# Kernel tuning notes

Hardware: AMD Instinct MI355X
Metric: run time of the kernel (lower is better)

Reference implementation:

```python
import jax, jax.numpy as jnp
import numpy as np

BN_EPS = 1e-5
C = 128  # channels (hardcoded by feed_forward convs)


def _bn(v, gamma, beta, mean, var):
    # BatchNorm1d in inference form over channel axis of [B, C, N]
    scale = gamma / jnp.sqrt(var + BN_EPS)
    return (v - mean[:, None]) * scale[:, None] + beta[:, None]


def setup_inputs() -> dict:
    key = jax.random.key(0)
    ks = jax.random.split(key, 8)
    B, N = 8, 2048
    s = 0.05
    return {
        "x": jax.random.normal(ks[0], (B, N, C), jnp.float32),
        "Wq": jax.random.normal(ks[1], (C // 4, C), jnp.float32) * s,
        "Wk": jax.random.normal(ks[2], (C // 4, C), jnp.float32) * s,
        "Wv": jax.random.normal(ks[3], (C, C), jnp.float32) * s,
        "bv": jnp.zeros((C,), jnp.float32),
        "Wt": jax.random.normal(ks[4], (C, C), jnp.float32) * s,
        "bt": jnp.zeros((C,), jnp.float32),
        "g1": jnp.ones((C,), jnp.float32),
        "b1": jnp.zeros((C,), jnp.float32),
        "m1": jnp.zeros((C,), jnp.float32),
        "v1": jnp.ones((C,), jnp.float32),
        "W1": jax.random.normal(ks[5], (512, C), jnp.float32) * s,
        "bf1": jnp.zeros((512,), jnp.float32),
        "W2": jax.random.normal(ks[6], (C, 512), jnp.float32) * s,
        "bf2": jnp.zeros((C,), jnp.float32),
        "g2": jnp.ones((C,), jnp.float32),
        "b2": jnp.zeros((C,), jnp.float32),
        "m2": jnp.zeros((C,), jnp.float32),
        "v2": jnp.ones((C,), jnp.float32),
    }


def reference(x, Wq, Wk, Wv, bv, Wt, bt, g1, b1, m1, v1,
              W1, bf1, W2, bf2, g2, b2, m2, v2):
    # x: [B, N, C] -> work in [B, C, N] layout like the torch module
    xc = jnp.transpose(x, (0, 2, 1))                      # [B, C, N]
    # q_conv(x).permute -> [B, N, C/4]; k_conv -> [B, C/4, N]
    x_q = jnp.einsum('bnc,oc->bno', x, Wq)                # [B, N, C/4]
    x_k = jnp.einsum('bnc,oc->bon', x, Wk)                # [B, C/4, N]
    x_v = jnp.einsum('bnc,oc->bon', x, Wv) + bv[:, None]  # [B, C, N]

    energy = jnp.einsum('bnd,bdm->bnm', x_q, x_k)         # [B, N, N]
    scale = jnp.sqrt(jnp.asarray(C, x.dtype))             # sqrt(x_v.shape[-2])
    attention = jax.nn.softmax(energy / scale, axis=-1)   # [B, N, N]
    x_r = jnp.einsum('bcn,bnm->bcm', x_v, attention)      # [B, C, N]

    t = jnp.einsum('oc,bcn->bon', Wt, xc - x_r) + bt[:, None]
    x_r2 = jax.nn.relu(_bn(t, g1, b1, m1, v1))
    h = xc + x_r2                                         # [B, C, N]

    residual = h
    f = jax.nn.relu(jnp.einsum('oc,bcn->bon', W1, h) + bf1[:, None])
    f = jnp.einsum('of,bfn->bon', W2, f) + bf2[:, None]
    out = _bn(residual + f, g2, b2, m2, v2)               # [B, C, N]
    return jnp.transpose(out, (0, 2, 1))                  # [B, N, C]
```

## Files before the change

kernel.cpp:

```cpp
#include <hip/hip_runtime.h>
#include <hip/hip_bf16.h>

#define BDIM 256
#define NPTS (8 * 2048)
#define CC 128
#define DD 32
#define FF 512
#define NN 2048
#define SCALE 0.08838834764831845f

typedef float f32x4 __attribute__((ext_vector_type(4)));
typedef short s16x8 __attribute__((ext_vector_type(8)));
typedef unsigned short ushort_t;

__device__ __forceinline__ ushort_t bf16r(float x) {
    __hip_bfloat16 h = __float2bfloat16(x);
    return *reinterpret_cast<ushort_t*>(&h);
}
__device__ __forceinline__ float bf16tof(ushort_t u) {
    unsigned v = ((unsigned)u) << 16;
    return *reinterpret_cast<float*>(&v);
}
__device__ __forceinline__ unsigned pack2(float a, float b) {
    return ((unsigned)bf16r(b) << 16) | (unsigned)bf16r(a);
}

__global__ void k_cvt_all(const float* __restrict__ W1, const float* __restrict__ W2,
                          const float* __restrict__ Wq, const float* __restrict__ Wk,
                          const float* __restrict__ Wv, const float* __restrict__ Wt,
                          ushort_t* __restrict__ dst) {
    int i = blockIdx.x * BDIM + threadIdx.x;
    const float* src; int off;
    if (i < 16384)      { src = W1; off = 0; }
    else if (i < 32768) { src = W2; off = 16384; }
    else if (i < 33792) { src = Wq; off = 32768; }
    else if (i < 34816) { src = Wk; off = 33792; }
    else if (i < 38912) { src = Wv; off = 34816; }
    else                { src = Wt; off = 38912; }
    float4 v = ((const float4*)src)[i - off];
    *(uint2*)(dst + (long)i * 4) = make_uint2(pack2(v.x, v.y), pack2(v.z, v.w));
}

__global__ __launch_bounds__(256) void k_proj(
        const float* __restrict__ x, const ushort_t* __restrict__ Wb,
        const float* __restrict__ bv,
        ushort_t* __restrict__ qg, ushort_t* __restrict__ kg,
        ushort_t* __restrict__ vTg) {
    __shared__ ushort_t xs[32][136];
    __shared__ ushort_t qks[32][72];
    __shared__ ushort_t vs[32][136];
    int b = blockIdx.x & 7;
    int n0 = (blockIdx.x >> 3) * 32;
    long base = (long)b * NN + n0;
    int t = threadIdx.x, w = t >> 6, l = t & 63, a = l & 15, g = l >> 4;
    {
        const float4* xg4 = (const float4*)(x + base * CC);
        #pragma unroll
        for (int rep = 0; rep < 4; ++rep) {
            int i = rep * BDIM + t;
            float4 v4 = xg4[i];
            int p = i >> 5, c4 = (i & 31) * 4;
            *(uint2*)&xs[p][c4] = make_uint2(pack2(v4.x, v4.y), pack2(v4.z, v4.w));
        }
    }
    s16x8 bF[3][4];
    #pragma unroll
    for (int ct = 0; ct < 3; ++ct) {
        int ctg = w * 3 + ct;
        #pragma unroll
        for (int ki = 0; ki < 4; ++ki)
            bF[ct][ki] = *(const s16x8*)(Wb + ((long)(ctg * 16 + a)) * CC + ki * 32 + g * 8);
    }
    __syncthreads();
    #pragma unroll
    for (int rt = 0; rt < 2; ++rt) {
        s16x8 aF[4];
        #pragma unroll
        for (int ki = 0; ki < 4; ++ki)
            aF[ki] = *(const s16x8*)&xs[rt * 16 + a][ki * 32 + g * 8];
        #pragma unroll
        for (int ct = 0; ct < 3; ++ct) {
            f32x4 acc = (f32x4){0.f, 0.f, 0.f, 0.f};
            #pragma unroll
            for (int ki = 0; ki < 4; ++ki)
                acc = __builtin_amdgcn_mfma_f32_16x16x32_bf16(aF[ki], bF[ct][ki], acc, 0, 0, 0);
            int ctg = w * 3 + ct;
            int oc = ctg * 16 + a;
            float bias = (oc >= 64) ? bv[oc - 64] : 0.f;
            #pragma unroll
            for (int r = 0; r < 4; ++r) {
                int p = rt * 16 + g * 4 + r;
                float val = acc[r] + bias;
                if (oc < 64) qks[p][oc] = bf16r(val);
                else         vs[p][oc - 64] = bf16r(val);
            }
        }
    }
    __syncthreads();
    {
        int p = t >> 3, c = (t & 7) * 4;
        *(uint2*)(qg + (base + p) * DD + c) = *(const uint2*)&qks[p][c];
        *(uint2*)(kg + (base + p) * DD + c) = *(const uint2*)&qks[p][32 + c];
    }
    #pragma unroll
    for (int rep = 0; rep < 2; ++rep) {
        int i = rep * BDIM + t;
        int c = i & 127, nch = i >> 7;
        int p0 = nch * 8;
        uint4 r;
        r.x = (unsigned)vs[p0+0][c] | ((unsigned)vs[p0+1][c] << 16);
        r.y = (unsigned)vs[p0+2][c] | ((unsigned)vs[p0+3][c] << 16);
        r.z = (unsigned)vs[p0+4][c] | ((unsigned)vs[p0+5][c] << 16);
        r.w = (unsigned)vs[p0+6][c] | ((unsigned)vs[p0+7][c] << 16);
        *(uint4*)(vTg + ((long)(b * CC + c)) * NN + n0 + p0) = r;
    }
}

__global__ __launch_bounds__(256) void k_rowstats(
        const ushort_t* __restrict__ qg, const ushort_t* __restrict__ kg,
        float* __restrict__ rowinv) {
    __shared__ float ps[4][64];
    int b = blockIdx.x & 7;
    int nt = (blockIdx.x >> 3) * 64;
    int t = threadIdx.x, w = t >> 6, l = t & 63, a = l & 15, g = l >> 4;
    s16x8 qA[4];
    #pragma unroll
    for (int s = 0; s < 4; ++s)
        qA[s] = *(const s16x8*)(qg + ((long)(b * NN + nt + s*16 + a)) * DD + g*8);
    float sm[16];
    #pragma unroll
    for (int i = 0; i < 16; ++i) sm[i] = 0.f;
    s16x8 kB = *(const s16x8*)(kg + ((long)(b * NN + w * 16 + a)) * DD + g*8);
    for (int it = 0; it < 32; ++it) {
        s16x8 kBn;
        if (it < 31)
            kBn = *(const s16x8*)(kg + ((long)(b * NN + ((it+1)*4 + w)*16 + a)) * DD + g*8);
        #pragma unroll
        for (int s = 0; s < 4; ++s) {
            f32x4 D = (f32x4){0.f, 0.f, 0.f, 0.f};
            D = __builtin_amdgcn_mfma_f32_16x16x32_bf16(qA[s], kB, D, 0, 0, 0);
            #pragma unroll
            for (int r = 0; r < 4; ++r)
                sm[s * 4 + r] += __expf(D[r] * SCALE);
        }
        kB = kBn;
    }
    #pragma unroll
    for (int off = 1; off < 16; off <<= 1)
        #pragma unroll
        for (int ix = 0; ix < 16; ++ix)
            sm[ix] += __shfl_xor(sm[ix], off, 64);
    if (a == 0) {
        #pragma unroll
        for (int s = 0; s < 4; ++s)
            #pragma unroll
            for (int r = 0; r < 4; ++r)
                ps[w][s * 16 + g * 4 + r] = sm[s * 4 + r];
    }
    __syncthreads();
    if (t < 64) {
        float S = ps[0][t] + ps[1][t] + ps[2][t] + ps[3][t];
        rowinv[(long)b * NN + nt + t] = 1.f / S;
    }
}

__global__ __launch_bounds__(512) void k_pv(
        const ushort_t* __restrict__ qg, const ushort_t* __restrict__ kg,
        const ushort_t* __restrict__ vTg, const float* __restrict__ rowinv,
        const float* __restrict__ x, const ushort_t* __restrict__ Wtb,
        const float* __restrict__ bt,
        const float* __restrict__ g1, const float* __restrict__ b1,
        const float* __restrict__ m1, const float* __restrict__ v1,
        ushort_t* __restrict__ hb) {
    __shared__ __align__(16) char arena[17408];
    auto pT = (ushort_t (*)[32][72])(arena);
    int b = blockIdx.x & 7;
    int m0 = (blockIdx.x >> 3) * 32;
    int t = threadIdx.x, w = t >> 6, l = t & 63, a = l & 15, g = l >> 4;
    int nsub = w & 3, msub = w >> 2;
    const ushort_t* vTb = vTg + (long)b * CC * NN;
    s16x8 kf = *(const s16x8*)(kg + ((long)(b * NN + m0 + msub * 16 + a)) * DD + g * 8);
    const ushort_t* qrow = qg + ((long)(b * NN + nsub * 16 + a)) * DD + g * 8;
    const float*    rrow = rowinv + (long)b * NN + nsub * 16 + g * 4;
    int c = w * 16 + a;
    const ushort_t* vrow = vTb + (long)c * NN + g * 8;
    s16x8 qf_c = *(const s16x8*)qrow;
    float4 rr_c = *(const float4*)rrow;
    s16x8 qf_n; float4 rr_n;
    s16x8 bf_use0, bf_use1, bf_ld0, bf_ld1;
    f32x4 acc[2];
    acc[0] = (f32x4){0.f, 0.f, 0.f, 0.f};
    acc[1] = (f32x4){0.f, 0.f, 0.f, 0.f};
    for (int it = 0; it <= 32; ++it) {
        if (it < 32) {
            f32x4 e = (f32x4){0.f, 0.f, 0.f, 0.f};
            e = __builtin_amdgcn_mfma_f32_16x16x32_bf16(qf_c, kf, e, 0, 0, 0);
            float p0 = __expf(e[0] * SCALE) * rr_c.x;
            float p1 = __expf(e[1] * SCALE) * rr_c.y;
            float p2 = __expf(e[2] * SCALE) * rr_c.z;
            float p3 = __expf(e[3] * SCALE) * rr_c.w;
            *(uint2*)&pT[it & 1][msub * 16 + a][nsub * 16 + g * 4] =
                make_uint2(pack2(p0, p1), pack2(p2, p3));
        }
        if (it < 31) {
            long off = (long)(it + 1) * 64;
            qf_n = *(const s16x8*)(qrow + off * DD);
            rr_n = *(const float4*)(rrow + off);
        }
        if (it < 32) {
            long off = (long)it * 64;
            bf_ld0 = *(const s16x8*)(vrow + off);
            bf_ld1 = *(const s16x8*)(vrow + off + 32);
        }
        if (it >= 1) {
            int pb = (it - 1) & 1;
            s16x8 A00 = *(const s16x8*)&pT[pb][a][g * 8];
            s16x8 A10 = *(const s16x8*)&pT[pb][16 + a][g * 8];
            s16x8 A01 = *(const s16x8*)&pT[pb][a][32 + g * 8];
            s16x8 A11 = *(const s16x8*)&pT[pb][16 + a][32 + g * 8];
            acc[0] = __builtin_amdgcn_mfma_f32_16x16x32_bf16(A00, bf_use0, acc[0], 0, 0, 0);
            acc[1] = __builtin_amdgcn_mfma_f32_16x16x32_bf16(A10, bf_use0, acc[1], 0, 0, 0);
            acc[0] = __builtin_amdgcn_mfma_f32_16x16x32_bf16(A01, bf_use1, acc[0], 0, 0, 0);
            acc[1] = __builtin_amdgcn_mfma_f32_16x16x32_bf16(A11, bf_use1, acc[1], 0, 0, 0);
        }
        bf_use0 = bf_ld0; bf_use1 = bf_ld1;
        qf_c = qf_n; rr_c = rr_n;
        __syncthreads();
    }
    auto xb  = (ushort_t (*)[136])(arena);
    auto dsx = (ushort_t (*)[136])(arena + 8704);
    long pbase = (long)b * NN + m0;
    {
        const float4* xg4 = (const float4*)(x + pbase * CC);
        #pragma unroll
        for (int rep = 0; rep < 2; ++rep) {
            int i = rep * 512 + t;
            float4 xv = xg4[i];
            int p = i >> 5, c4 = (i & 31) * 4;
            *(uint2*)&xb[p][c4] = make_uint2(pack2(xv.x, xv.y), pack2(xv.z, xv.w));
        }
    }
    __syncthreads();
    #pragma unroll
    for (int ms = 0; ms < 2; ++ms)
        #pragma unroll
        for (int r = 0; r < 4; ++r) {
            int ml = ms * 16 + g * 4 + r;
            dsx[ml][c] = bf16r(bf16tof(xb[ml][c]) - acc[ms][r]);
        }
    __syncthreads();
    {
        int ph = w & 1, fh = w >> 1;
        s16x8 aF[4];
        #pragma unroll
        for (int ki = 0; ki < 4; ++ki)
            aF[ki] = *(const s16x8*)&dsx[ph * 16 + a][ki * 32 + g * 8];
        #pragma unroll
        for (int oi = 0; oi < 2; ++oi) {
            int ot = fh * 2 + oi;
            f32x4 ac = (f32x4){0.f, 0.f, 0.f, 0.f};
            #pragma unroll
            for (int ki = 0; ki < 4; ++ki) {
                s16x8 bF = *(const s16x8*)(Wtb + ((long)(ot * 16 + a)) * CC + ki * 32 + g * 8);
                ac = __builtin_amdgcn_mfma_f32_16x16x32_bf16(aF[ki], bF, ac, 0, 0, 0);
            }
            int o = ot * 16 + a;
            float sc = g1[o] * rsqrtf(v1[o] + 1e-5f);
            float mm = m1[o], bb = b1[o], bo = bt[o];
            #pragma unroll
            for (int r = 0; r < 4; ++r) {
                int p = ph * 16 + g * 4 + r;
                float tv = ((ac[r] + bo) - mm) * sc + bb;
                tv = fmaxf(tv, 0.f);
                hb[(pbase + p) * CC + o] = bf16r(bf16tof(xb[p][o]) + tv);
            }
        }
    }
}

__global__ __launch_bounds__(256) void k_ff(
        const ushort_t* __restrict__ hb, const ushort_t* __restrict__ W1b,
        const ushort_t* __restrict__ W2b,
        const float* __restrict__ bf1, const float* __restrict__ bf2,
        const float* __restrict__ g2, const float* __restrict__ b2,
        const float* __restrict__ m2, const float* __restrict__ v2,
        float* __restrict__ out) {
    __shared__ ushort_t hs[32][136];
    __shared__ ushort_t w1s[2][64][128];
    __shared__ ushort_t w2s[2][128][64];
    __shared__ ushort_t fss[32][72];
    long pbase = (long)(blockIdx.x & 7) * NN + (blockIdx.x >> 3) * 32;
    int t = threadIdx.x;
    int l = t & 63, wid = t >> 6;
    int ph = wid & 1, fh = wid >> 1;
    int lr = l & 15, lg = l >> 4;
    for (int i = t; i < 512; i += BDIM) {
        int r = i >> 4, c0 = (i & 15) * 8;
        *(uint4*)&hs[r][c0] = *(const uint4*)(hb + (pbase + r) * CC + c0);
    }
    #pragma unroll
    for (int rep = 0; rep < 4; ++rep) {
        int i = rep * BDIM + t;
        int r = i >> 4, c0 = (i & 15) * 8;
        *(uint4*)&w1s[0][r][c0 ^ ((r & 7) * 8)] = *(const uint4*)(W1b + (long)r * CC + c0);
    }
    #pragma unroll
    for (int rep = 0; rep < 4; ++rep) {
        int i = rep * BDIM + t;
        int r = i >> 3, c0 = (i & 7) * 8;
        *(uint4*)&w2s[0][r][c0 ^ ((r & 7) * 8)] = *(const uint4*)(W2b + (long)r * FF + c0);
    }
    __syncthreads();
    s16x8 hA[4];
    #pragma unroll
    for (int ki = 0; ki < 4; ++ki)
        hA[ki] = *(const s16x8*)&hs[ph * 16 + lr][ki * 32 + lg * 8];
    f32x4 acc2[4];
    #pragma unroll
    for (int i = 0; i < 4; ++i) acc2[i] = (f32x4){0.f, 0.f, 0.f, 0.f};

    int cur = 0;
    uint4 wrg0, wrg1, wrg2, wrg3, wrg4, wrg5, wrg6, wrg7;
    for (int fc = 0; fc < 8; ++fc) {
        if (fc) __syncthreads();
        int f0 = fc * 64;
        if (fc < 7) {
            int f0n = f0 + 64;
            int r1 = t >> 4, c1 = (t & 15) * 8;
            int r2 = t >> 3, c2 = (t & 7) * 8;
            wrg0 = *(const uint4*)(W1b + (long)(f0n + r1) * CC + c1);
            wrg1 = *(const uint4*)(W1b + (long)(f0n + 16 + r1) * CC + c1);
            wrg2 = *(const uint4*)(W1b + (long)(f0n + 32 + r1) * CC + c1);
            wrg3 = *(const uint4*)(W1b + (long)(f0n + 48 + r1) * CC + c1);
            wrg4 = *(const uint4*)(W2b + (long)r2 * FF + f0n + c2);
            wrg5 = *(const uint4*)(W2b + (long)(32 + r2) * FF + f0n + c2);
            wrg6 = *(const uint4*)(W2b + (long)(64 + r2) * FF + f0n + c2);
            wrg7 = *(const uint4*)(W2b + (long)(96 + r2) * FF + f0n + c2);
        }
        #pragma unroll
        for (int fi = 0; fi < 2; ++fi) {
            int ft = fh * 2 + fi;
            int row = ft * 16 + lr;
            f32x4 a1 = (f32x4){0.f, 0.f, 0.f, 0.f};
            #pragma unroll
            for (int ki = 0; ki < 4; ++ki) {
                int col = ki * 32 + lg * 8;
                s16x8 bfr = *(const s16x8*)&w1s[cur][row][col ^ ((row & 7) * 8)];
                a1 = __builtin_amdgcn_mfma_f32_16x16x32_bf16(hA[ki], bfr, a1, 0, 0, 0);
            }
            float bias = bf1[f0 + ft * 16 + lr];
            #pragma unroll
            for (int r = 0; r < 4; ++r) {
                float vv = fmaxf(a1[r] + bias, 0.f);
                fss[ph * 16 + lg * 4 + r][ft * 16 + lr] = bf16r(vv);
            }
        }
        __syncthreads();
        #pragma unroll
        for (int k2 = 0; k2 < 2; ++k2) {
            s16x8 afr = *(const s16x8*)&fss[ph * 16 + lr][k2 * 32 + lg * 8];
            #pragma unroll
            for (int oi = 0; oi < 4; ++oi) {
                int ot = fh * 4 + oi;
                int row = ot * 16 + lr;
                int col = k2 * 32 + lg * 8;
                s16x8 bfr = *(const s16x8*)&w2s[cur][row][col ^ ((row & 7) * 8)];
                acc2[oi] = __builtin_amdgcn_mfma_f32_16x16x32_bf16(afr, bfr, acc2[oi], 0, 0, 0);
            }
        }
        if (fc < 7) {
            int nb = cur ^ 1;
            int r1 = t >> 4, c1 = (t & 15) * 8;
            int r2 = t >> 3, c2 = (t & 7) * 8;
            *(uint4*)&w1s[nb][r1][c1 ^ ((r1 & 7) * 8)] = wrg0;
            *(uint4*)&w1s[nb][16 + r1][c1 ^ ((r1 & 7) * 8)] = wrg1;
            *(uint4*)&w1s[nb][32 + r1][c1 ^ ((r1 & 7) * 8)] = wrg2;
            *(uint4*)&w1s[nb][48 + r1][c1 ^ ((r1 & 7) * 8)] = wrg3;
            *(uint4*)&w2s[nb][r2][c2 ^ ((r2 & 7) * 8)] = wrg4;
            *(uint4*)&w2s[nb][32 + r2][c2 ^ (((32 + r2) & 7) * 8)] = wrg5;
            *(uint4*)&w2s[nb][64 + r2][c2 ^ (((64 + r2) & 7) * 8)] = wrg6;
            *(uint4*)&w2s[nb][96 + r2][c2 ^ (((96 + r2) & 7) * 8)] = wrg7;
            cur = nb;
        }
    }
    #pragma unroll
    for (int oi = 0; oi < 4; ++oi) {
        int o = (fh * 4 + oi) * 16 + lr;
        float sc = g2[o] * rsqrtf(v2[o] + 1e-5f);
        float mm = m2[o], bb = b2[o], bias2 = bf2[o];
        #pragma unroll
        for (int r = 0; r < 4; ++r) {
            int p = ph * 16 + lg * 4 + r;
            float val = bf16tof(hs[p][o]) + acc2[oi][r] + bias2;
            out[(pbase + p) * CC + o] = (val - mm) * sc + bb;
        }
    }
}

extern "C" void kernel_launch(void* const* d_in, const int* in_sizes, int n_in,
                              void* d_out, int out_size, void* d_ws, size_t ws_size,
                              hipStream_t stream) {
    const float* x   = (const float*)d_in[0];
    const float* Wq  = (const float*)d_in[1];
    const float* Wk  = (const float*)d_in[2];
    const float* Wv  = (const float*)d_in[3];
    const float* bv  = (const float*)d_in[4];
    const float* Wt  = (const float*)d_in[5];
    const float* bt  = (const float*)d_in[6];
    const float* g1  = (const float*)d_in[7];
    const float* b1  = (const float*)d_in[8];
    const float* m1  = (const float*)d_in[9];
    const float* v1  = (const float*)d_in[10];
    const float* W1  = (const float*)d_in[11];
    const float* bf1 = (const float*)d_in[12];
    const float* W2  = (const float*)d_in[13];
    const float* bf2 = (const float*)d_in[14];
    const float* g2  = (const float*)d_in[15];
    const float* b2  = (const float*)d_in[16];
    const float* m2  = (const float*)d_in[17];
    const float* v2  = (const float*)d_in[18];
    float* out = (float*)d_out;

    float* ws  = (float*)d_ws;
    float* rin = ws;
    ushort_t* qg   = (ushort_t*)(rin + NPTS);
    ushort_t* kg   = qg + (long)NPTS * DD;
    ushort_t* vTg  = kg + (long)NPTS * DD;
    ushort_t* hbuf = vTg + (long)NPTS * CC;
    ushort_t* W1b  = hbuf + (long)NPTS * CC;
    ushort_t* W2b  = W1b + FF * CC;
    ushort_t* Wb   = W2b + FF * CC;
    ushort_t* Wtb  = Wb + 192 * CC;

    k_cvt_all<<<168, BDIM, 0, stream>>>(W1, W2, Wq, Wk, Wv, Wt, W1b);
    k_proj<<<NPTS / 32, BDIM, 0, stream>>>(x, Wb, bv, qg, kg, vTg);
    k_rowstats<<<8 * (NN / 64), BDIM, 0, stream>>>(qg, kg, rin);
    k_pv<<<8 * (NN / 32), 512, 0, stream>>>(qg, kg, vTg, rin,
                                            x, Wtb, bt, g1, b1, m1, v1, hbuf);
    k_ff<<<NPTS / 32, BDIM, 0, stream>>>(hbuf, W1b, W2b, bf1, bf2, g2, b2, m2, v2, out);
}
```

Measured before the change: 85.01 us.

## Stage V tiles through double-buffered LDS with cooperative coalesced loads in PV kernel

Instead of each wave reading its V^T fragments directly from global memory, the block cooperatively loads each 128x64 V tile into a double-buffered shared-memory array and reads MFMA operands from LDS. The P tile becomes single-buffered with an extra barrier between its write and the MFMA reads. This aims to improve global load coalescing and overlap next-tile loads with compute. In exchange it raises LDS usage, which may lower occupancy, and adds a barrier per iteration.

Measured after the change: 70.41 us (median of 4 runs). -17.2%, faster.

```diff
diff --git a/kernel.cpp b/kernel.cpp
--- a/kernel.cpp
+++ b/kernel.cpp
@@ -172,8 +172,9 @@
         const float* __restrict__ g1, const float* __restrict__ b1,
         const float* __restrict__ m1, const float* __restrict__ v1,
         ushort_t* __restrict__ hb) {
-    __shared__ __align__(16) char arena[17408];
-    auto pT = (ushort_t (*)[32][72])(arena);
+    __shared__ __align__(16) char arena[41472];
+    auto vTs = (ushort_t (*)[128][72])(arena);
+    auto pT  = (ushort_t (*)[72])(arena + 36864);
     int b = blockIdx.x & 7;
     int m0 = (blockIdx.x >> 3) * 32;
     int t = threadIdx.x, w = t >> 6, l = t & 63, a = l & 15, g = l >> 4;
@@ -182,50 +183,56 @@
     s16x8 kf = *(const s16x8*)(kg + ((long)(b * NN + m0 + msub * 16 + a)) * DD + g * 8);
     const ushort_t* qrow = qg + ((long)(b * NN + nsub * 16 + a)) * DD + g * 8;
     const float*    rrow = rowinv + (long)b * NN + nsub * 16 + g * 4;
-    int c = w * 16 + a;
-    const ushort_t* vrow = vTb + (long)c * NN + g * 8;
+    int sc = t >> 3;
+    int sj = (t & 7) * 8;
     s16x8 qf_c = *(const s16x8*)qrow;
     float4 rr_c = *(const float4*)rrow;
-    s16x8 qf_n; float4 rr_n;
-    s16x8 bf_use0, bf_use1, bf_ld0, bf_ld1;
+    {
+        uint4 v0 = *(const uint4*)(vTb + (long)sc * NN + sj);
+        uint4 v1 = *(const uint4*)(vTb + (long)(64 + sc) * NN + sj);
+        *(uint4*)&vTs[0][sc][sj] = v0;
+        *(uint4*)&vTs[0][64 + sc][sj] = v1;
+    }
     f32x4 acc[2];
     acc[0] = (f32x4){0.f, 0.f, 0.f, 0.f};
     acc[1] = (f32x4){0.f, 0.f, 0.f, 0.f};
-    for (int it = 0; it <= 32; ++it) {
-        if (it < 32) {
+    int cur = 0;
+    __syncthreads();
+    s16x8 qf_n; float4 rr_n; uint4 vsr0, vsr1;
+    for (int it = 0; it < 32; ++it) {
+        long ntn = (long)(it + 1) * 64;
+        if (it < 31) {
+            vsr0 = *(const uint4*)(vTb + (long)sc * NN + ntn + sj);
+            vsr1 = *(const uint4*)(vTb + (long)(64 + sc) * NN + ntn + sj);
+            qf_n = *(const s16x8*)(qrow + ntn * DD);
+            rr_n = *(const float4*)(rrow + ntn);
+        }
+        {
             f32x4 e = (f32x4){0.f, 0.f, 0.f, 0.f};
             e = __builtin_amdgcn_mfma_f32_16x16x32_bf16(qf_c, kf, e, 0, 0, 0);
             float p0 = __expf(e[0] * SCALE) * rr_c.x;
             float p1 = __expf(e[1] * SCALE) * rr_c.y;
             float p2 = __expf(e[2] * SCALE) * rr_c.z;
             float p3 = __expf(e[3] * SCALE) * rr_c.w;
-            *(uint2*)&pT[it & 1][msub * 16 + a][nsub * 16 + g * 4] =
+            *(uint2*)&pT[msub * 16 + a][nsub * 16 + g * 4] =
                 make_uint2(pack2(p0, p1), pack2(p2, p3));
         }
+        __syncthreads();
+        #pragma unroll
+        for (int k2 = 0; k2 < 2; ++k2) {
+            s16x8 A0 = *(const s16x8*)&pT[a][k2 * 32 + g * 8];
+            s16x8 A1 = *(const s16x8*)&pT[16 + a][k2 * 32 + g * 8];
+            s16x8 Bf = *(const s16x8*)&vTs[cur][w * 16 + a][k2 * 32 + g * 8];
+            acc[0] = __builtin_amdgcn_mfma_f32_16x16x32_bf16(A0, Bf, acc[0], 0, 0, 0);
+            acc[1] = __builtin_amdgcn_mfma_f32_16x16x32_bf16(A1, Bf, acc[1], 0, 0, 0);
+        }
         if (it < 31) {
-            long off = (long)(it + 1) * 64;
-            qf_n = *(const s16x8*)(qrow + off * DD);
-            rr_n = *(const float4*)(rrow + off);
-        }
-        if (it < 32) {
-            long off = (long)it * 64;
-            bf_ld0 = *(const s16x8*)(vrow + off);
-            bf_ld1 = *(const s16x8*)(vrow + off + 32);
-        }
-        if (it >= 1) {
-            int pb = (it - 1) & 1;
-            s16x8 A00 = *(const s16x8*)&pT[pb][a][g * 8];
-            s16x8 A10 = *(const s16x8*)&pT[pb][16 + a][g * 8];
-            s16x8 A01 = *(const s16x8*)&pT[pb][a][32 + g * 8];
-            s16x8 A11 = *(const s16x8*)&pT[pb][16 + a][32 + g * 8];
-            acc[0] = __builtin_amdgcn_mfma_f32_16x16x32_bf16(A00, bf_use0, acc[0], 0, 0, 0);
-            acc[1] = __builtin_amdgcn_mfma_f32_16x16x32_bf16(A10, bf_use0, acc[1], 0, 0, 0);
-            acc[0] = __builtin_amdgcn_mfma_f32_16x16x32_bf16(A01, bf_use1, acc[0], 0, 0, 0);
-            acc[1] = __builtin_amdgcn_mfma_f32_16x16x32_bf16(A11, bf_use1, acc[1], 0, 0, 0);
-        }
-        bf_use0 = bf_ld0; bf_use1 = bf_ld1;
+            *(uint4*)&vTs[cur ^ 1][sc][sj] = vsr0;
+            *(uint4*)&vTs[cur ^ 1][64 + sc][sj] = vsr1;
+        }
         qf_c = qf_n; rr_c = rr_n;
         __syncthreads();
+        cur ^= 1;
     }
     auto xb  = (ushort_t (*)[136])(arena);
     auto dsx = (ushort_t (*)[136])(arena + 8704);
@@ -241,13 +248,16 @@
         }
     }
     __syncthreads();
-    #pragma unroll
-    for (int ms = 0; ms < 2; ++ms)
-        #pragma unroll
-        for (int r = 0; r < 4; ++r) {
-            int ml = ms * 16 + g * 4 + r;
-            dsx[ml][c] = bf16r(bf16tof(xb[ml][c]) - acc[ms][r]);
-        }
+    {
+        int c = w * 16 + a;
+        #pragma unroll
+        for (int ms = 0; ms < 2; ++ms)
+            #pragma unroll
+            for (int r = 0; r < 4; ++r) {
+                int ml = ms * 16 + g * 4 + r;
+                dsx[ml][c] = bf16r(bf16tof(xb[ml][c]) - acc[ms][r]);
+            }
+    }
     __syncthreads();
     {
         int ph = w & 1, fh = w >> 1;
```
